# Kernel optimization log

Measured on AMD Instinct MI355X. Metric: run time of the kernel, lower is better.

Reference implementation:

```python
import jax, jax.numpy as jnp
import numpy as np

B, N = 16, 512            # graphs per batch, nodes per graph
V, D_EMB = 100000, 64     # embedding table
F0 = 64                   # raw node feature width
H = 8                     # heads per layer
F_IN0 = F0 + D_EMB + 3    # 131 after concat(emb)+concat(user_emb)
O1, O2 = 128, 128         # f_out of layer 0 and 1
F_IN1 = H * O1            # 1024
EPS = 1e-5


def _xavier(key, shape):
    fan_in, fan_out = shape[-2], shape[-1]
    lim = float(np.sqrt(6.0 / (fan_in + fan_out)))
    return jax.random.uniform(key, shape, jnp.float32, -lim, lim)


def setup_inputs() -> dict:
    key = jax.random.key(0)
    ks = jax.random.split(key, 16)
    vertices = jax.random.randint(ks[0], (B, N), 0, V)
    adj = (jax.random.uniform(ks[1], (B, N, N)) < 0.1).astype(jnp.float32)
    adj = jnp.maximum(adj, jnp.eye(N, dtype=jnp.float32))  # self-loops: no empty softmax rows
    h = jax.random.normal(ks[2], (B, N, F0), jnp.float32)
    user_emb = jax.random.normal(ks[3], (B, N, 3), jnp.float32)
    emb_table = jax.random.normal(ks[4], (V, D_EMB), jnp.float32)
    return {
        "vertices": vertices, "adj": adj, "h": h, "user_emb": user_emb,
        "emb_table": emb_table,
        "norm1_w": jnp.ones((D_EMB,), jnp.float32), "norm1_b": jnp.zeros((D_EMB,), jnp.float32),
        "norm2_w": jnp.ones((3,), jnp.float32), "norm2_b": jnp.zeros((3,), jnp.float32),
        "w0": _xavier(ks[5], (H, F_IN0, O1)),
        "a_src0": _xavier(ks[6], (H, O1, 1)), "a_dst0": _xavier(ks[7], (H, O1, 1)),
        "w1": _xavier(ks[8], (H, F_IN1, O2)),
        "a_src1": _xavier(ks[9], (H, O2, 1)), "a_dst1": _xavier(ks[10], (H, O2, 1)),
    }


def _instance_norm(x, w, b):
    # torch InstanceNorm1d on x.transpose(1,2): normalize over node dim per (batch, channel)
    mu = jnp.mean(x, axis=1, keepdims=True)
    var = jnp.var(x, axis=1, keepdims=True)  # biased variance, as torch
    return (x - mu) * jax.lax.rsqrt(var + EPS) * w + b


def _gat_layer(h, adj, w, a_src, a_dst):
    # h: [b,n,f_in], w: [h,f_in,o]
    hp = jnp.einsum('bnf,hfo->bhno', h, w)            # h_prime
    t = jnp.tanh(hp)
    s = jnp.einsum('bhno,ho->bhn', t, a_src[..., 0])  # attn_src
    d = jnp.einsum('bhno,ho->bhn', t, a_dst[..., 0])  # attn_dst
    attn = s[:, :, :, None] + d[:, :, None, :]        # [b,h,n,n]
    attn = jnp.where(attn >= 0, attn, 0.2 * attn)     # leaky_relu(0.2)
    attn = jnp.where(adj[:, None, :, :] > 0, attn, -jnp.inf)
    attn = jax.nn.softmax(attn, axis=-1)              # (dropout is identity in eval)
    return jnp.einsum('bhnm,bhmo->bhno', attn, hp)


def reference(vertices, adj, h, user_emb, emb_table,
              norm1_w, norm1_b, norm2_w, norm2_b,
              w0, a_src0, a_dst0, w1, a_src1, a_dst1):
    emb = emb_table[vertices]                         # [b,n,D_EMB]
    emb = _instance_norm(emb, norm1_w, norm1_b)
    x = jnp.concatenate([h, emb], axis=2)
    ue = _instance_norm(user_emb, norm2_w, norm2_b)
    x = jnp.concatenate([x, ue], axis=2)              # [b,n,F_IN0]
    # layer 0 (not last): elu + head concat
    x = _gat_layer(x, adj, w0, a_src0, a_dst0)        # [b,H,n,O1]
    x = jax.nn.elu(jnp.transpose(x, (0, 2, 1, 3)).reshape(B, N, H * O1))
    # layer 1 (last): mean over heads
    x = _gat_layer(x, adj, w1, a_src1, a_dst1)        # [b,H,n,O2]
    x = jnp.mean(x, axis=1)                           # [b,n,O2]
    return jax.nn.log_softmax(x, axis=-1)
```

## Files before the change

kernel.cpp:

```cpp
#include <hip/hip_runtime.h>
#include <hip/hip_bf16.h>
#include <cmath>

#define B_  16
#define N_  512
#define H_  8
#define F0_ 64
#define DEMB_ 64
#define FIN0_ 131
#define KP0_ 192
#define O_  128
#define FIN1_ 1024
#define LOG2E_ 1.4426950408889634f

typedef __attribute__((ext_vector_type(4))) float f32x4;
typedef __attribute__((ext_vector_type(8))) short bf16x8;

__device__ inline ushort f2bf(float f) {
    union { float f; unsigned u; } x; x.f = f;
    unsigned r = x.u + 0x7fff + ((x.u >> 16) & 1);
    return (ushort)(r >> 16);
}
__device__ inline float bf2f(ushort u) {
    union { unsigned u; float f; } x; x.u = ((unsigned)u) << 16;
    return x.f;
}
__device__ inline float tanh_fast(float x) {
    x = fminf(fmaxf(x, -15.f), 15.f);
    float e = __expf(2.f * x);
    return (e - 1.f) * __frcp_rn(e + 1.f);
}

__global__ __launch_bounds__(256) void k_pre(const float* __restrict__ h,
                                             const int* __restrict__ verts,
                                             const float* __restrict__ table,
                                             const float* __restrict__ n1w,
                                             const float* __restrict__ n1b,
                                             const float* __restrict__ ue,
                                             const float* __restrict__ n2w,
                                             const float* __restrict__ n2b,
                                             const float* __restrict__ w0,
                                             const float* __restrict__ w1,
                                             const float* __restrict__ adj,
                                             ushort* __restrict__ x0,
                                             ushort* __restrict__ wt0,
                                             ushort* __restrict__ wt1,
                                             unsigned long long* __restrict__ mask) {
    __shared__ float s0[256], s1[256];
    int bid = blockIdx.x;
    int t = threadIdx.x;

    if (bid < 2048) {
        int i = bid * 256 + t;
        int r = i >> 6, c = i & 63;
        x0[(size_t)r * KP0_ + c] = f2bf(h[i]);
        if (c >= 3) x0[(size_t)r * KP0_ + 128 + c] = 0;
    } else if (bid < 3072) {
        int b2 = bid - 2048;
        int b = b2 >> 6, c = b2 & 63;
        float vals[2], sum = 0.f, sq = 0.f;
#pragma unroll
        for (int i = 0; i < 2; ++i) {
            int n = t + i * 256;
            int vid = verts[b * N_ + n];
            float v = table[(size_t)vid * DEMB_ + c];
            vals[i] = v; sum += v; sq += v * v;
        }
        s0[t] = sum; s1[t] = sq; __syncthreads();
        for (int o = 128; o > 0; o >>= 1) {
            if (t < o) { s0[t] += s0[t + o]; s1[t] += s1[t + o]; }
            __syncthreads();
        }
        float mu = s0[0] * (1.f / N_);
        float var = s1[0] * (1.f / N_) - mu * mu;
        float inv = rsqrtf(var + 1e-5f);
        float ww = n1w[c], bv = n1b[c];
#pragma unroll
        for (int i = 0; i < 2; ++i) {
            int n = t + i * 256;
            x0[((size_t)b * N_ + n) * KP0_ + 64 + c] = f2bf((vals[i] - mu) * inv * ww + bv);
        }
    } else if (bid < 3120) {
        int b3 = bid - 3072;
        int b = b3 / 3, c = b3 % 3;
        float vals[2], sum = 0.f, sq = 0.f;
#pragma unroll
        for (int i = 0; i < 2; ++i) {
            int n = t + i * 256;
            float v = ue[((size_t)b * N_ + n) * 3 + c];
            vals[i] = v; sum += v; sq += v * v;
        }
        s0[t] = sum; s1[t] = sq; __syncthreads();
        for (int o = 128; o > 0; o >>= 1) {
            if (t < o) { s0[t] += s0[t + o]; s1[t] += s1[t + o]; }
            __syncthreads();
        }
        float mu = s0[0] * (1.f / N_);
        float var = s1[0] * (1.f / N_) - mu * mu;
        float inv = rsqrtf(var + 1e-5f);
        float ww = n2w[c], bv = n2b[c];
#pragma unroll
        for (int i = 0; i < 2; ++i) {
            int n = t + i * 256;
            x0[((size_t)b * N_ + n) * KP0_ + 128 + c] = f2bf((vals[i] - mu) * inv * ww + bv);
        }
    } else if (bid < 3728) {
        int ob = (bid - 3120) * 2 + (t >> 7);
        int o = t & 127;
        if (ob < 192) {
            int hh = ob / 24, kc = ob % 24;
            bf16x8 v;
#pragma unroll
            for (int j = 0; j < 8; ++j) {
                int k = kc * 8 + j;
                float f = (k < FIN0_) ? w0[((size_t)hh * FIN0_ + k) * 128 + o] : 0.f;
                v[j] = (short)f2bf(f);
            }
            *(bf16x8*)(wt0 + ((size_t)(hh * 128 + o)) * KP0_ + kc * 8) = v;
        } else {
            int b2 = ob - 192;
            int hh = b2 >> 7, kc = b2 & 127;
            bf16x8 v;
#pragma unroll
            for (int j = 0; j < 8; ++j) {
                int k = kc * 8 + j;
                float f = w1[((size_t)hh * FIN1_ + k) * 128 + o];
                v[j] = (short)f2bf(f);
            }
            *(bf16x8*)(wt1 + ((size_t)(hh * 128 + o)) * FIN1_ + kc * 8) = v;
        }
    } else {
        int gid = (bid - 3728) * 256 + t;
        float v = adj[gid];
        unsigned long long m = __ballot(v > 0.f);
        if ((t & 63) == 0) mask[gid >> 6] = m;
    }
}

template <int K>
__global__ __launch_bounds__(256, 2) void k_gemm(const ushort* __restrict__ A,
                                                 const ushort* __restrict__ Wt,
                                                 const float* __restrict__ asrc,
                                                 const float* __restrict__ adst,
                                                 ushort* __restrict__ hpT,
                                                 float* __restrict__ sout,
                                                 float* __restrict__ dout) {
    __shared__ ushort As[128 * 64];
    __shared__ ushort Bs[128 * 64];
    int bid = blockIdx.x;
    int idx = bid >> 3;
    int mt = (bid & 7) + 8 * (idx & 7);
    int hh = idx >> 3;
    int tid = threadIdx.x;
    int wid = tid >> 6, l = tid & 63;
    int wm = wid >> 1, wn = wid & 1;

    const ushort* Ab = A + (size_t)mt * 128 * K;
    const ushort* Wb = Wt + (size_t)hh * 128 * K;

    f32x4 acc[4][4];
#pragma unroll
    for (int m = 0; m < 4; ++m)
#pragma unroll
        for (int n = 0; n < 4; ++n) acc[m][n] = (f32x4){0.f, 0.f, 0.f, 0.f};

    int srow = tid >> 3;
    int segp = tid & 7;

    for (int kt = 0; kt < K / 64; ++kt) {
        int k0 = kt * 64;
#pragma unroll
        for (int it = 0; it < 4; ++it) {
            int row = it * 32 + srow;
            int segl = segp ^ (row & 7);
            size_t goff = (size_t)row * K + k0 + segl * 8;
            int loff = (it * 32 + wid * 8) * 64;
            __builtin_amdgcn_global_load_lds(
                (const __attribute__((address_space(1))) void*)(Ab + goff),
                (__attribute__((address_space(3))) void*)(As + loff), 16, 0, 0);
            __builtin_amdgcn_global_load_lds(
                (const __attribute__((address_space(1))) void*)(Wb + goff),
                (__attribute__((address_space(3))) void*)(Bs + loff), 16, 0, 0);
        }
        __syncthreads();

        int lr = l & 15;
        int kg = l >> 4;
#pragma unroll
        for (int kk = 0; kk < 2; ++kk) {
            int segl = kk * 4 + kg;
            bf16x8 a[4], b[4];
#pragma unroll
            for (int m = 0; m < 4; ++m) {
                int row = wm * 64 + m * 16 + lr;
                int sp = segl ^ (row & 7);
                a[m] = *(const bf16x8*)(As + row * 64 + sp * 8);
            }
#pragma unroll
            for (int n = 0; n < 4; ++n) {
                int row = wn * 64 + n * 16 + lr;
                int sp = segl ^ (row & 7);
                b[n] = *(const bf16x8*)(Bs + row * 64 + sp * 8);
            }
#pragma unroll
            for (int m = 0; m < 4; ++m)
#pragma unroll
                for (int n = 0; n < 4; ++n)
                    acc[m][n] = __builtin_amdgcn_mfma_f32_16x16x32_bf16(a[m], b[n], acc[m][n], 0, 0, 0);
        }
        __syncthreads();
    }

    int bb = mt >> 2;
    int n_in_b = (mt & 3) * 128;
    int bh = bb * H_ + hh;
    ushort* Hp = hpT + ((size_t)bh * 128) * 512;
#pragma unroll
    for (int m = 0; m < 4; ++m)
#pragma unroll
        for (int n = 0; n < 4; ++n) {
            int rr = wm * 64 + m * 16 + (l >> 4) * 4;
            int cc = wn * 64 + n * 16 + (l & 15);
            ushort4 v;
            v.x = f2bf(acc[m][n][0]);
            v.y = f2bf(acc[m][n][1]);
            v.z = f2bf(acc[m][n][2]);
            v.w = f2bf(acc[m][n][3]);
            *(ushort4*)(Hp + (size_t)cc * 512 + n_in_b + rr) = v;
        }

    float* sP = (float*)As;
    float* dP = sP + 256;
    float av[4], dv[4];
#pragma unroll
    for (int n = 0; n < 4; ++n) {
        int cc = wn * 64 + n * 16 + (l & 15);
        av[n] = asrc[hh * 128 + cc];
        dv[n] = adst[hh * 128 + cc];
    }
#pragma unroll
    for (int m = 0; m < 4; ++m)
#pragma unroll
        for (int j = 0; j < 4; ++j) {
            float sv = 0.f, dvv = 0.f;
#pragma unroll
            for (int n = 0; n < 4; ++n) {
                float th = tanh_fast(acc[m][n][j]);
                sv += th * av[n];
                dvv += th * dv[n];
            }
#pragma unroll
            for (int off = 1; off < 16; off <<= 1) {
                sv += __shfl_xor(sv, off);
                dvv += __shfl_xor(dvv, off);
            }
            if ((l & 15) == 0) {
                int rr = wm * 64 + m * 16 + (l >> 4) * 4 + j;
                sP[wn * 128 + rr] = sv;
                dP[wn * 128 + rr] = dvv;
            }
        }
    __syncthreads();
    if (tid < 128) {
        sout[(size_t)bh * 512 + n_in_b + tid] = (sP[tid] + sP[128 + tid]) * LOG2E_;
    } else {
        int r = tid - 128;
        dout[(size_t)bh * 512 + n_in_b + r] = (dP[r] + dP[128 + r]) * LOG2E_;
    }
}

template <bool L0>
__global__ __launch_bounds__(256, 2) void k_attn(const ushort* __restrict__ hpT,
                                                 const float* __restrict__ sbuf,
                                                 const float* __restrict__ dbuf,
                                                 const unsigned* __restrict__ mask32,
                                                 ushort* __restrict__ out) {
    __shared__ ushort Vbuf[2][128 * 64];
    __shared__ ushort Abuf[64 * 64];
    __shared__ float dsh[512];
    __shared__ float rsh[64];

    int bid = blockIdx.x;
    int xcd = bid & 7, idx = bid >> 3;
    int bh = xcd + 8 * (idx & 15);
    int tile = idx >> 4;
    int b = bh >> 3, hh = bh & 7;
    int n0 = tile * 64;
    int t = threadIdx.x;
    int wid = t >> 6, l = t & 63;
    int wm = wid >> 1, wn = wid & 1;
    int lr = l & 15, kg = l >> 4;

    const ushort* Vb = hpT + (size_t)bh * 128 * 512;

    int row = t >> 2, q4 = t & 3;
    float sv = sbuf[(size_t)bh * 512 + n0 + row];
    int msh = (q4 & 1) * 16;
    unsigned mw[8];
#pragma unroll
    for (int c = 0; c < 8; ++c)
        mw[c] = mask32[((size_t)(b * 512 + n0 + row) << 4) + c * 2 + (q4 >> 1)];

    int srow = t >> 3, segp = t & 7;

#pragma unroll
    for (int it = 0; it < 4; ++it) {
        int rrow = it * 32 + srow;
        int segl = segp ^ (rrow & 7);
        __builtin_amdgcn_global_load_lds(
            (const __attribute__((address_space(1))) void*)(Vb + (size_t)rrow * 512 + segl * 8),
            (__attribute__((address_space(3))) void*)(Vbuf[0] + (it * 32 + wid * 8) * 64),
            16, 0, 0);
    }

    dsh[t] = dbuf[(size_t)bh * 512 + t];
    dsh[256 + t] = dbuf[(size_t)bh * 512 + 256 + t];

    f32x4 acc[4][2];
#pragma unroll
    for (int m = 0; m < 4; ++m)
#pragma unroll
        for (int n = 0; n < 2; ++n) acc[m][n] = (f32x4){0.f, 0.f, 0.f, 0.f};

    float rsum = 0.f;
    __syncthreads();

#pragma unroll
    for (int c = 0; c < 8; ++c) {
        int m0 = c * 64;

        const float* dp = dsh + m0 + q4 * 16;
        unsigned mwc = mw[c] >> msh;
#pragma unroll
        for (int j = 0; j < 2; ++j) {
            f32x4 da = *(const f32x4*)(dp + j * 8);
            f32x4 db2 = *(const f32x4*)(dp + j * 8 + 4);
            float ev[8];
#pragma unroll
            for (int q = 0; q < 8; ++q) {
                float dm = (q < 4) ? da[q] : db2[q - 4];
                float lg = sv + dm;
                lg = fmaxf(lg, 0.2f * lg);
                float e = ((mwc >> (j * 8 + q)) & 1) ? exp2f(lg) : 0.f;
                rsum += e;
                ev[q] = e;
            }
            unsigned p01, p23, p45, p67;
            asm("v_cvt_pk_bf16_f32 %0, %1, %2" : "=v"(p01) : "v"(ev[0]), "v"(ev[1]));
            asm("v_cvt_pk_bf16_f32 %0, %1, %2" : "=v"(p23) : "v"(ev[2]), "v"(ev[3]));
            asm("v_cvt_pk_bf16_f32 %0, %1, %2" : "=v"(p45) : "v"(ev[4]), "v"(ev[5]));
            asm("v_cvt_pk_bf16_f32 %0, %1, %2" : "=v"(p67) : "v"(ev[6]), "v"(ev[7]));
            int s = q4 * 2 + j;
            int phys = s ^ (row & 7);
            uint4 pk4 = {p01, p23, p45, p67};
            *(uint4*)((char*)Abuf + row * 128 + phys * 16) = pk4;
        }
        __syncthreads();

        const ushort* Vcur = Vbuf[c & 1];
#pragma unroll
        for (int kk = 0; kk < 2; ++kk) {
            int s = kk * 4 + kg;
            bf16x8 a[4], bfr[2];
#pragma unroll
            for (int m = 0; m < 4; ++m) {
                int rw = wm * 64 + m * 16 + lr;
                int sp = s ^ (rw & 7);
                a[m] = *(const bf16x8*)(Vcur + rw * 64 + sp * 8);
            }
#pragma unroll
            for (int n = 0; n < 2; ++n) {
                int rw = wn * 32 + n * 16 + lr;
                int sp = s ^ (rw & 7);
                bfr[n] = *(const bf16x8*)(Abuf + rw * 64 + sp * 8);
            }
#pragma unroll
            for (int m = 0; m < 4; ++m)
#pragma unroll
                for (int n = 0; n < 2; ++n)
                    acc[m][n] = __builtin_amdgcn_mfma_f32_16x16x32_bf16(a[m], bfr[n], acc[m][n], 0, 0, 0);
        }
        __syncthreads();

        if (c < 7) {
            int m1 = (c + 1) * 64;
            ushort* Vnxt = Vbuf[(c + 1) & 1];
#pragma unroll
            for (int it = 0; it < 4; ++it) {
                int rrow = it * 32 + srow;
                int segl = segp ^ (rrow & 7);
                __builtin_amdgcn_global_load_lds(
                    (const __attribute__((address_space(1))) void*)(Vb + (size_t)rrow * 512 + m1 + segl * 8),
                    (__attribute__((address_space(3))) void*)(Vnxt + (it * 32 + wid * 8) * 64),
                    16, 0, 0);
            }
        }
    }

    rsum += __shfl_xor(rsum, 1);
    rsum += __shfl_xor(rsum, 2);
    if (q4 == 0) rsh[row] = rsum;
    __syncthreads();

#pragma unroll
    for (int n = 0; n < 2; ++n) {
        int nn = wn * 32 + n * 16 + lr;
        float ri = __frcp_rn(rsh[nn]);
        size_t orow;
        if (L0)
            orow = ((size_t)(b * 512 + n0 + nn)) * FIN1_ + hh * 128;
        else
            orow = ((size_t)bh * 512 + n0 + nn) * 128;
#pragma unroll
        for (int m = 0; m < 4; ++m) {
            int o0 = wm * 64 + m * 16 + kg * 4;
            f32x4 v = acc[m][n];
            ushort4 w;
            float f0 = v[0] * ri, f1 = v[1] * ri, f2 = v[2] * ri, f3 = v[3] * ri;
            if (L0) {
                f0 = (f0 > 0.f) ? f0 : expm1f(f0);
                f1 = (f1 > 0.f) ? f1 : expm1f(f1);
                f2 = (f2 > 0.f) ? f2 : expm1f(f2);
                f3 = (f3 > 0.f) ? f3 : expm1f(f3);
            }
            w.x = f2bf(f0); w.y = f2bf(f1); w.z = f2bf(f2); w.w = f2bf(f3);
            *(ushort4*)(out + orow + o0) = w;
        }
    }
}

__global__ __launch_bounds__(128) void k_out(const ushort* __restrict__ o1,
                                             float* __restrict__ out) {
    int row = blockIdx.x;
    int b = row >> 9, n = row & 511;
    int t = threadIdx.x;
    float v = 0.f;
#pragma unroll
    for (int hh = 0; hh < H_; ++hh)
        v += bf2f(o1[((size_t)(b * H_ + hh) * N_ + n) * O_ + t]);
    v *= 0.125f;
    float m = v;
#pragma unroll
    for (int off = 32; off > 0; off >>= 1) m = fmaxf(m, __shfl_down(m, off));
    __shared__ float red[4];
    if ((t & 63) == 0) red[t >> 6] = m;
    __syncthreads();
    float rm = fmaxf(red[0], red[1]);
    float e = __expf(v - rm);
    float ss = e;
#pragma unroll
    for (int off = 32; off > 0; off >>= 1) ss += __shfl_down(ss, off);
    if ((t & 63) == 0) red[2 + (t >> 6)] = ss;
    __syncthreads();
    float rs2 = red[2] + red[3];
    out[(size_t)row * O_ + t] = v - rm - logf(rs2);
}

extern "C" void kernel_launch(void* const* d_in, const int* in_sizes, int n_in,
                              void* d_out, int out_size, void* d_ws, size_t ws_size,
                              hipStream_t stream) {
    const int*   verts = (const int*)d_in[0];
    const float* adj   = (const float*)d_in[1];
    const float* h     = (const float*)d_in[2];
    const float* ue    = (const float*)d_in[3];
    const float* table = (const float*)d_in[4];
    const float* n1w   = (const float*)d_in[5];
    const float* n1b   = (const float*)d_in[6];
    const float* n2w   = (const float*)d_in[7];
    const float* n2b   = (const float*)d_in[8];
    const float* w0    = (const float*)d_in[9];
    const float* as0   = (const float*)d_in[10];
    const float* ad0   = (const float*)d_in[11];
    const float* w1    = (const float*)d_in[12];
    const float* as1   = (const float*)d_in[13];
    const float* ad1   = (const float*)d_in[14];
    float* out = (float*)d_out;

    ushort* x0p  = (ushort*)d_ws;
    ushort* wt0  = x0p + 1572864;
    ushort* wt1  = wt0 + 196608;
    ushort* hpT  = wt1 + 1048576;
    ushort* x1bf = hpT + 8388608;
    ushort* o1   = x1bf + 8388608;
    unsigned long long* mask = (unsigned long long*)(o1 + 8388608);
    float* sb = (float*)(mask + 65536);
    float* db = sb + 65536;

    hipLaunchKernelGGL(k_pre, dim3(20112), dim3(256), 0, stream,
                       h, verts, table, n1w, n1b, ue, n2w, n2b, w0, w1, adj,
                       x0p, wt0, wt1, mask);

    hipLaunchKernelGGL((k_gemm<KP0_>), dim3(512), dim3(256), 0, stream,
                       x0p, wt0, as0, ad0, hpT, sb, db);
    hipLaunchKernelGGL((k_attn<true>), dim3(1024), dim3(256), 0, stream,
                       hpT, sb, db, (const unsigned*)mask, x1bf);

    hipLaunchKernelGGL((k_gemm<FIN1_>), dim3(512), dim3(256), 0, stream,
                       x1bf, wt1, as1, ad1, hpT, sb, db);
    hipLaunchKernelGGL((k_attn<false>), dim3(1024), dim3(256), 0, stream,
                       hpT, sb, db, (const unsigned*)mask, o1);

    hipLaunchKernelGGL(k_out, dim3(8192), dim3(128), 0, stream, o1, out);
}
```

Baseline: 120.6 us.

## Compute attention probabilities in registers as MFMA B operand, drop Abuf LDS staging

Restructures the attention kernel so each wave owns 16 query rows and builds its bf16 exp-probability fragment directly in registers, feeding it straight into the MFMA as the B operand. This removes the Abuf shared staging, one barrier per chunk, and the cross-wave row-sum reduction through shared memory. Launch bounds move to 4 blocks per CU. The cost is that each wave now reads all 128 V rows from LDS, which adds LDS read traffic, and it holds more mask words per thread.

```diff
diff --git a/kernel.cpp b/kernel.cpp
--- a/kernel.cpp
+++ b/kernel.cpp
@@ -270,15 +270,13 @@
 }
 
 template <bool L0>
-__global__ __launch_bounds__(256, 2) void k_attn(const ushort* __restrict__ hpT,
+__global__ __launch_bounds__(256, 4) void k_attn(const ushort* __restrict__ hpT,
                                                  const float* __restrict__ sbuf,
                                                  const float* __restrict__ dbuf,
                                                  const unsigned* __restrict__ mask32,
                                                  ushort* __restrict__ out) {
     __shared__ ushort Vbuf[2][128 * 64];
-    __shared__ ushort Abuf[64 * 64];
     __shared__ float dsh[512];
-    __shared__ float rsh[64];
 
     int bid = blockIdx.x;
     int xcd = bid & 7, idx = bid >> 3;
@@ -288,18 +286,16 @@
     int n0 = tile * 64;
     int t = threadIdx.x;
     int wid = t >> 6, l = t & 63;
-    int wm = wid >> 1, wn = wid & 1;
     int lr = l & 15, kg = l >> 4;
 
     const ushort* Vb = hpT + (size_t)bh * 128 * 512;
 
-    int row = t >> 2, q4 = t & 3;
-    float sv = sbuf[(size_t)bh * 512 + n0 + row];
-    int msh = (q4 & 1) * 16;
-    unsigned mw[8];
-#pragma unroll
-    for (int c = 0; c < 8; ++c)
-        mw[c] = mask32[((size_t)(b * 512 + n0 + row) << 4) + c * 2 + (q4 >> 1)];
+    int nn = n0 + wid * 16 + lr;
+    float sv = sbuf[(size_t)bh * 512 + nn];
+    unsigned mw[16];
+#pragma unroll
+    for (int w = 0; w < 16; ++w)
+        mw[w] = mask32[((size_t)(b * 512 + nn) << 4) + w];
 
     int srow = t >> 3, segp = t & 7;
 
@@ -312,74 +308,16 @@
             (__attribute__((address_space(3))) void*)(Vbuf[0] + (it * 32 + wid * 8) * 64),
             16, 0, 0);
     }
-
     dsh[t] = dbuf[(size_t)bh * 512 + t];
     dsh[256 + t] = dbuf[(size_t)bh * 512 + 256 + t];
 
-    f32x4 acc[4][2];
-#pragma unroll
-    for (int m = 0; m < 4; ++m)
-#pragma unroll
-        for (int n = 0; n < 2; ++n) acc[m][n] = (f32x4){0.f, 0.f, 0.f, 0.f};
-
+    f32x4 acc[8];
+#pragma unroll
+    for (int f = 0; f < 8; ++f) acc[f] = (f32x4){0.f, 0.f, 0.f, 0.f};
     float rsum = 0.f;
-    __syncthreads();
 
 #pragma unroll
     for (int c = 0; c < 8; ++c) {
-        int m0 = c * 64;
-
-        const float* dp = dsh + m0 + q4 * 16;
-        unsigned mwc = mw[c] >> msh;
-#pragma unroll
-        for (int j = 0; j < 2; ++j) {
-            f32x4 da = *(const f32x4*)(dp + j * 8);
-            f32x4 db2 = *(const f32x4*)(dp + j * 8 + 4);
-            float ev[8];
-#pragma unroll
-            for (int q = 0; q < 8; ++q) {
-                float dm = (q < 4) ? da[q] : db2[q - 4];
-                float lg = sv + dm;
-                lg = fmaxf(lg, 0.2f * lg);
-                float e = ((mwc >> (j * 8 + q)) & 1) ? exp2f(lg) : 0.f;
-                rsum += e;
-                ev[q] = e;
-            }
-            unsigned p01, p23, p45, p67;
-            asm("v_cvt_pk_bf16_f32 %0, %1, %2" : "=v"(p01) : "v"(ev[0]), "v"(ev[1]));
-            asm("v_cvt_pk_bf16_f32 %0, %1, %2" : "=v"(p23) : "v"(ev[2]), "v"(ev[3]));
-            asm("v_cvt_pk_bf16_f32 %0, %1, %2" : "=v"(p45) : "v"(ev[4]), "v"(ev[5]));
-            asm("v_cvt_pk_bf16_f32 %0, %1, %2" : "=v"(p67) : "v"(ev[6]), "v"(ev[7]));
-            int s = q4 * 2 + j;
-            int phys = s ^ (row & 7);
-            uint4 pk4 = {p01, p23, p45, p67};
-            *(uint4*)((char*)Abuf + row * 128 + phys * 16) = pk4;
-        }
-        __syncthreads();
-
-        const ushort* Vcur = Vbuf[c & 1];
-#pragma unroll
-        for (int kk = 0; kk < 2; ++kk) {
-            int s = kk * 4 + kg;
-            bf16x8 a[4], bfr[2];
-#pragma unroll
-            for (int m = 0; m < 4; ++m) {
-                int rw = wm * 64 + m * 16 + lr;
-                int sp = s ^ (rw & 7);
-                a[m] = *(const bf16x8*)(Vcur + rw * 64 + sp * 8);
-            }
-#pragma unroll
-            for (int n = 0; n < 2; ++n) {
-                int rw = wn * 32 + n * 16 + lr;
-                int sp = s ^ (rw & 7);
-                bfr[n] = *(const bf16x8*)(Abuf + rw * 64 + sp * 8);
-            }
-#pragma unroll
-            for (int m = 0; m < 4; ++m)
-#pragma unroll
-                for (int n = 0; n < 2; ++n)
-                    acc[m][n] = __builtin_amdgcn_mfma_f32_16x16x32_bf16(a[m], bfr[n], acc[m][n], 0, 0, 0);
-        }
         __syncthreads();
 
         if (c < 7) {
@@ -395,37 +333,66 @@
                     16, 0, 0);
             }
         }
-    }
-
-    rsum += __shfl_xor(rsum, 1);
-    rsum += __shfl_xor(rsum, 2);
-    if (q4 == 0) rsh[row] = rsum;
-    __syncthreads();
-
-#pragma unroll
-    for (int n = 0; n < 2; ++n) {
-        int nn = wn * 32 + n * 16 + lr;
-        float ri = __frcp_rn(rsh[nn]);
-        size_t orow;
-        if (L0)
-            orow = ((size_t)(b * 512 + n0 + nn)) * FIN1_ + hh * 128;
-        else
-            orow = ((size_t)bh * 512 + n0 + nn) * 128;
-#pragma unroll
-        for (int m = 0; m < 4; ++m) {
-            int o0 = wm * 64 + m * 16 + kg * 4;
-            f32x4 v = acc[m][n];
-            ushort4 w;
-            float f0 = v[0] * ri, f1 = v[1] * ri, f2 = v[2] * ri, f3 = v[3] * ri;
-            if (L0) {
-                f0 = (f0 > 0.f) ? f0 : expm1f(f0);
-                f1 = (f1 > 0.f) ? f1 : expm1f(f1);
-                f2 = (f2 > 0.f) ? f2 : expm1f(f2);
-                f3 = (f3 > 0.f) ? f3 : expm1f(f3);
-            }
-            w.x = f2bf(f0); w.y = f2bf(f1); w.z = f2bf(f2); w.w = f2bf(f3);
-            *(ushort4*)(out + orow + o0) = w;
-        }
+
+        const ushort* Vcur = Vbuf[c & 1];
+#pragma unroll
+        for (int ks = 0; ks < 2; ++ks) {
+            const float* dp = dsh + c * 64 + ks * 32 + kg * 8;
+            f32x4 da = *(const f32x4*)dp;
+            f32x4 db2 = *(const f32x4*)(dp + 4);
+            unsigned mwc = mw[c * 2 + ks] >> (kg * 8);
+            float ev[8];
+#pragma unroll
+            for (int q = 0; q < 8; ++q) {
+                float dm = (q < 4) ? da[q] : db2[q - 4];
+                float lg = sv + dm;
+                lg = fmaxf(lg, 0.2f * lg);
+                float e = ((mwc >> q) & 1) ? exp2f(lg) : 0.f;
+                rsum += e;
+                ev[q] = e;
+            }
+            unsigned p01, p23, p45, p67;
+            asm("v_cvt_pk_bf16_f32 %0, %1, %2" : "=v"(p01) : "v"(ev[0]), "v"(ev[1]));
+            asm("v_cvt_pk_bf16_f32 %0, %1, %2" : "=v"(p23) : "v"(ev[2]), "v"(ev[3]));
+            asm("v_cvt_pk_bf16_f32 %0, %1, %2" : "=v"(p45) : "v"(ev[4]), "v"(ev[5]));
+            asm("v_cvt_pk_bf16_f32 %0, %1, %2" : "=v"(p67) : "v"(ev[6]), "v"(ev[7]));
+            union { uint4 u; bf16x8 h; } pk;
+            pk.u = (uint4){p01, p23, p45, p67};
+
+            int s = ks * 4 + kg;
+#pragma unroll
+            for (int f = 0; f < 8; ++f) {
+                int rw = f * 16 + lr;
+                int sp = s ^ (rw & 7);
+                bf16x8 a = *(const bf16x8*)(Vcur + rw * 64 + sp * 8);
+                acc[f] = __builtin_amdgcn_mfma_f32_16x16x32_bf16(a, pk.h, acc[f], 0, 0, 0);
+            }
+        }
+    }
+
+    rsum += __shfl_xor(rsum, 16);
+    rsum += __shfl_xor(rsum, 32);
+    float ri = __frcp_rn(rsum);
+
+    size_t orow;
+    if (L0)
+        orow = ((size_t)(b * 512 + nn)) * FIN1_ + hh * 128;
+    else
+        orow = ((size_t)bh * 512 + nn) * 128;
+#pragma unroll
+    for (int f = 0; f < 8; ++f) {
+        int o0 = f * 16 + kg * 4;
+        f32x4 v = acc[f];
+        ushort4 w;
+        float f0 = v[0] * ri, f1 = v[1] * ri, f2 = v[2] * ri, f3 = v[3] * ri;
+        if (L0) {
+            f0 = (f0 > 0.f) ? f0 : expm1f(f0);
+            f1 = (f1 > 0.f) ? f1 : expm1f(f1);
+            f2 = (f2 > 0.f) ? f2 : expm1f(f2);
+            f3 = (f3 > 0.f) ? f3 : expm1f(f3);
+        }
+        w.x = f2bf(f0); w.y = f2bf(f1); w.z = f2bf(f2); w.w = f2bf(f3);
+        *(ushort4*)(out + orow + o0) = w;
     }
 }
 
```

Measured after the change: 135.0 us. +12.0%, slower.
